# Kernel tuning notes

Measured on AMD Instinct MI355X. Metric: run time of the kernel, lower is better.

Reference implementation:

```python
import jax, jax.numpy as jnp
import numpy as np

EPS_CB = 1e-6   # ConvBlock BN eps (partial(nn.BatchNorm2d, eps=1e-6))
EPS_BN = 1e-5   # default nn.BatchNorm2d / BatchNorm1d eps


def conv2d(x, w, stride=1, pad=0):
    return jax.lax.conv_general_dilated(
        x, w, (stride, stride), [(pad, pad), (pad, pad)],
        dimension_numbers=('NCHW', 'OIHW', 'NCHW'))


def bn2d(x, g, b, m, v, eps):
    inv = (g / jnp.sqrt(v + eps)).reshape(1, -1, 1, 1)
    return (x - m.reshape(1, -1, 1, 1)) * inv + b.reshape(1, -1, 1, 1)


def setup_inputs() -> dict:
    key = jax.random.key(0)
    ks = iter(jax.random.split(key, 40))
    B, C, H, W = 16, 512, 64, 64
    K = 64                 # num_codes (hard-coded to 64 in __init__)
    c4 = C // 4            # bottleneck width in ConvBlock (expansion=4)

    def w_(shape, scale=0.05):
        return jax.random.normal(next(ks), shape, jnp.float32) * scale

    def bnp(n):
        return (jax.random.uniform(next(ks), (n,), jnp.float32, 0.5, 1.5),  # gamma
                w_((n,), 0.05),                                            # beta
                w_((n,), 0.05),                                            # running mean
                jax.random.uniform(next(ks), (n,), jnp.float32, 0.5, 1.5)) # running var

    g1, b1, m1, v1 = bnp(c4)
    g2, b2, m2, v2 = bnp(c4)
    g3, b3, m3, v3 = bnp(C)
    gr, br, mr, vr = bnp(C)
    gl, bl, ml, vl = bnp(C)
    ge, be, me, ve = bnp(K)

    std = 1.0 / np.sqrt(K * C)
    inp = {
        'x': jax.random.normal(next(ks), (B, C, H, W), jnp.float32),
        # ConvBlock
        'w1': w_((c4, C, 1, 1)), 'g1': g1, 'b1': b1, 'm1': m1, 'v1': v1,
        'w2': w_((c4, c4, 3, 3)), 'g2': g2, 'b2': b2, 'm2': m2, 'v2': v2,
        'w3': w_((C, c4, 1, 1)), 'g3': g3, 'b3': b3, 'm3': m3, 'v3': v3,
        'wr': w_((C, C, 1, 1)), 'gr': gr, 'br': br, 'mr': mr, 'vr': vr,
        # LVC 1x1 conv + BN2d
        'wl': w_((C, C, 1, 1)), 'gl': gl, 'bl': bl, 'ml': ml, 'vl': vl,
        # Encoding
        'codewords': jax.random.uniform(next(ks), (K, C), jnp.float32, -std, std),
        'scale': jax.random.uniform(next(ks), (K,), jnp.float32, -1.0, 0.0),
        # BN1d over codes
        'ge': ge, 'be': be, 'me': me, 've': ve,
        # fc gate
        'wfc': w_((C, C)), 'bfc': w_((C,), 0.05),
    }
    return inp


def lvc_forward(x, w1, g1, b1, m1, v1, w2, g2, b2, m2, v2, w3, g3, b3, m3, v3,
                wr, gr, br, mr, vr, wl, gl, bl, ml, vl, codewords, scale,
                ge, be, me, ve, wfc, bfc):
    # ---- ConvBlock (bottleneck with 1x1 residual), eval-mode BN ----
    h = jax.nn.relu(bn2d(conv2d(x, w1), g1, b1, m1, v1, EPS_CB))
    h = jax.nn.relu(bn2d(conv2d(h, w2, pad=1), g2, b2, m2, v2, EPS_CB))
    h = jax.nn.relu(bn2d(conv2d(h, w3), g3, b3, m3, v3, EPS_CB))
    res = bn2d(conv2d(x, wr), gr, br, mr, vr, EPS_CB)
    x1 = h + res                                   # (B, C, H, W)

    # ---- LVC: 1x1 conv + BN + ReLU ----
    y = jax.nn.relu(bn2d(conv2d(x1, wl), gl, bl, ml, vl, EPS_BN))

    # ---- Encoding: scaled L2 -> softmax over codes -> aggregate ----
    B, C, H, W = y.shape
    xf = y.reshape(B, C, H * W).transpose(0, 2, 1)     # (B, N, C)
    x_sq = jnp.sum(xf * xf, axis=-1, keepdims=True)    # (B, N, 1)
    c_sq = jnp.sum(codewords * codewords, axis=-1)     # (K,)
    xc = jnp.einsum('bnc,kc->bnk', xf, codewords)      # (B, N, K)
    dist = scale * (x_sq - 2.0 * xc + c_sq)            # (B, N, K)
    A = jax.nn.softmax(dist, axis=2)                   # assignment weights
    # sum_n A[b,n,k] * (x[b,n,:] - codewords[k,:])  -> (B, K, C)
    enc = jnp.einsum('bnk,bnc->bkc', A, xf) - A.sum(axis=1)[..., None] * codewords

    # ---- BN1d over num_codes dim + ReLU + mean over codes ----
    inv = (ge / jnp.sqrt(ve + EPS_BN)).reshape(1, -1, 1)
    enc = (enc - me.reshape(1, -1, 1)) * inv + be.reshape(1, -1, 1)
    en = jax.nn.relu(enc).mean(axis=1)                 # (B, C)

    # ---- SE-style gate ----
    gam = jax.nn.sigmoid(en @ wfc.T + bfc)             # (B, C)
    gate = gam.reshape(B, C, 1, 1)
    return jax.nn.relu(x1 + x1 * gate)


def reference(x, w1, g1, b1, m1, v1, w2, g2, b2, m2, v2, w3, g3, b3, m3, v3,
              wr, gr, br, mr, vr, wl, gl, bl, ml, vl, codewords, scale,
              ge, be, me, ve, wfc, bfc):
    return lvc_forward(x, w1, g1, b1, m1, v1, w2, g2, b2, m2, v2,
                       w3, g3, b3, m3, v3, wr, gr, br, mr, vr,
                       wl, gl, bl, ml, vl, codewords, scale,
                       ge, be, me, ve, wfc, bfc)
```

## Files before the change

kernel.cpp:

```cpp
#include <hip/hip_runtime.h>
#include <math.h>

typedef float f32x4 __attribute__((ext_vector_type(4)));
typedef short s16x8 __attribute__((ext_vector_type(8)));
typedef unsigned short u16x4 __attribute__((ext_vector_type(4)));

#define HW 4096
#define CCH 512
#define NK 64
#define EPAD 136

#define C_XB   0ULL
#define C_H2   67108864ULL
#define C_H1P  83886080ULL
#define C_X1B  83886080ULL
#define C_YB   0ULL
#define C_AHI  67108864ULL
#define C_ALO  75497472ULL
#define C_ASUM 150994944ULL
#define C_GAM  150999040ULL
#define C_MISC 151031808ULL
#define C_W1F  151048192ULL
#define C_W2F  151179264ULL
#define C_W3B  151474176ULL
#define C_WRB  151605248ULL
#define C_WLB  152129536ULL
#define C_PE   152653824ULL

#define MS_S1 0
#define MS_T1 128
#define MS_S2 256
#define MS_T2 384
#define MS_S3 512
#define MS_T3 1024
#define MS_SR 1536
#define MS_TR 2048
#define MS_SL 2560
#define MS_TL 3072
#define MS_SE 3584
#define MS_TE 3648
#define MS_CSQ 3712

__device__ __forceinline__ float b2f(unsigned short u) {
  unsigned int x = ((unsigned int)u) << 16;
  return __builtin_bit_cast(float, x);
}
__device__ __forceinline__ unsigned short f2b(float f) {
  unsigned int i = __builtin_bit_cast(unsigned int, f);
  i += 0x7fffu + ((i >> 16) & 1u);
  return (unsigned short)(i >> 16);
}

__device__ __forceinline__ void gload16(const void* g, void* l) {
  __builtin_amdgcn_global_load_lds((const __attribute__((address_space(1))) void*)g,
                                   (__attribute__((address_space(3))) void*)l, 16, 0, 0);
}

__global__ void prep_kernel(
    const float* __restrict__ g1, const float* __restrict__ b1, const float* __restrict__ m1, const float* __restrict__ v1,
    const float* __restrict__ g2, const float* __restrict__ b2, const float* __restrict__ m2, const float* __restrict__ v2,
    const float* __restrict__ g3, const float* __restrict__ b3, const float* __restrict__ m3, const float* __restrict__ v3,
    const float* __restrict__ gr, const float* __restrict__ br, const float* __restrict__ mr, const float* __restrict__ vr,
    const float* __restrict__ gl, const float* __restrict__ bl, const float* __restrict__ ml, const float* __restrict__ vl,
    const float* __restrict__ ge, const float* __restrict__ be, const float* __restrict__ me, const float* __restrict__ ve,
    const float* __restrict__ cw, float* __restrict__ misc)
{
  const int t = threadIdx.x;
  if (t < 128) {
    float s = g1[t] * rsqrtf(v1[t] + 1e-6f);
    misc[MS_S1 + t] = s; misc[MS_T1 + t] = b1[t] - m1[t] * s;
    s = g2[t] * rsqrtf(v2[t] + 1e-6f);
    misc[MS_S2 + t] = s; misc[MS_T2 + t] = b2[t] - m2[t] * s;
  }
  for (int c = t; c < 512; c += 256) {
    float s = g3[c] * rsqrtf(v3[c] + 1e-6f);
    misc[MS_S3 + c] = s; misc[MS_T3 + c] = b3[c] - m3[c] * s;
    s = gr[c] * rsqrtf(vr[c] + 1e-6f);
    misc[MS_SR + c] = s; misc[MS_TR + c] = br[c] - mr[c] * s;
    s = gl[c] * rsqrtf(vl[c] + 1e-5f);
    misc[MS_SL + c] = s; misc[MS_TL + c] = bl[c] - ml[c] * s;
  }
  if (t < 64) {
    float s = ge[t] * rsqrtf(ve[t] + 1e-5f);
    misc[MS_SE + t] = s; misc[MS_TE + t] = be[t] - me[t] * s;
    float acc = 0.f;
    for (int c = 0; c < 512; ++c) { float v = cw[t * 512 + c]; acc += v * v; }
    misc[MS_CSQ + t] = acc;
  }
}

__global__ void fold_bf16_kernel(const float* __restrict__ w, const float* __restrict__ s,
                                 unsigned short* __restrict__ out, int total, int kper)
{
  int i = blockIdx.x * 256 + threadIdx.x;
  if (i < total) out[i] = f2b(w[i] * s[i / kper]);
}

__global__ void fold_w2_kernel(const float* __restrict__ w2, const float* __restrict__ s,
                               unsigned short* __restrict__ out)
{
  int j = blockIdx.x * 256 + threadIdx.x;
  if (j < 147456) {
    int m = j / 1152, r = j - m * 1152;
    int tp = r >> 7, ci = r & 127;
    out[j] = f2b(w2[m * 1152 + ci * 9 + tp] * s[m]);
  }
}

__global__ __launch_bounds__(256) void tr_kernel(const float* __restrict__ x,
                                                 unsigned short* __restrict__ xb)
{
  __shared__ float T[64][65];
  const int b = blockIdx.z, c0 = blockIdx.y * 64, n0 = blockIdx.x * 64;
  const int t = threadIdx.x;
  const int rr = t >> 4, cc = (t & 15) * 4;
#pragma unroll
  for (int rep = 0; rep < 4; ++rep) {
    const int cr = rep * 16 + rr;
    const float4 v = *(const float4*)(x + ((size_t)(b * 512 + c0 + cr)) * 4096 + n0 + cc);
    T[cr][cc + 0] = v.x; T[cr][cc + 1] = v.y; T[cr][cc + 2] = v.z; T[cr][cc + 3] = v.w;
  }
  __syncthreads();
#pragma unroll
  for (int rep = 0; rep < 4; ++rep) {
    const int nr = rep * 16 + rr;
    u16x4 o;
    o[0] = f2b(T[cc + 0][nr]); o[1] = f2b(T[cc + 1][nr]);
    o[2] = f2b(T[cc + 2][nr]); o[3] = f2b(T[cc + 3][nr]);
    *(u16x4*)(xb + ((size_t)(b * 4096 + n0 + nr)) * 512 + c0 + cc) = o;
  }
}


__device__ __forceinline__ void mfma_step(const unsigned short* __restrict__ Ac,
                                          const unsigned short* __restrict__ Bc,
                                          int lane, int wm, int wn, f32x4 acc[4][4])
{
  s16x8 afr[4], bfr[4];
#pragma unroll
  for (int i = 0; i < 4; ++i)
    afr[i] = *(const s16x8*)(Ac + (size_t)((wm * 4 + i) * 64 + lane) * 8);
#pragma unroll
  for (int j = 0; j < 4; ++j)
    bfr[j] = *(const s16x8*)(Bc + (size_t)((wn * 4 + j) * 64 + lane) * 8);
#pragma unroll
  for (int i = 0; i < 4; ++i)
#pragma unroll
    for (int j = 0; j < 4; ++j)
      acc[i][j] = __builtin_amdgcn_mfma_f32_16x16x32_bf16(afr[i], bfr[j], acc[i][j], 0, 0, 0);
}

template<int BMODE>
__device__ __forceinline__ void run_phase(
    const unsigned short* __restrict__ Wp,
    const unsigned short* __restrict__ Xb,
    const int K, const int tid, const int n0,
    unsigned short* __restrict__ As, unsigned short* __restrict__ Bs,
    f32x4 acc[4][4])
{
  const int lane = tid & 63;
  const int wv = tid >> 6, wm = wv >> 1, wn = wv & 1;

  const int row0 = (tid >> 6) * 16 + (tid & 15);
  const int row1 = row0 + 64;
  const int kofs = ((tid >> 4) & 3) * 8;

  const unsigned short* aS0 = Wp + (size_t)row0 * K + kofs;
  const unsigned short* aS1 = Wp + (size_t)row1 * K + kofs;

  const unsigned short* bS0 = nullptr;
  const unsigned short* bS1 = nullptr;
  size_t bBase0 = 0, bBase1 = 0;
  if constexpr (BMODE == 0) {
    bS0 = Xb + (size_t)(n0 + row0) * K + kofs;
    bS1 = Xb + (size_t)(n0 + row1) * K + kofs;
  } else {
    const int pg0 = n0 + row0, pg1 = n0 + row1;
    bBase0 = (size_t)((pg0 >> 6) * 66 + (pg0 & 63)) * 128 + kofs;
    bBase1 = (size_t)((pg1 >> 6) * 66 + (pg1 & 63)) * 128 + kofs;
  }

  const int wb = __builtin_amdgcn_readfirstlane(wv * 1024);

#define STAGE(kt, buf)                                            \
  {                                                               \
    char* aD = (char*)As + (buf) * 8192 + wb;                     \
    char* bD = (char*)Bs + (buf) * 8192 + wb;                     \
    if constexpr (BMODE == 0) {                                   \
      gload16(aS0 + (kt), aD);                                    \
      gload16(aS1 + (kt), aD + 4096);                             \
      gload16(bS0 + (kt), bD);                                    \
      gload16(bS1 + (kt), bD + 4096);                             \
    } else {                                                      \
      const int tap_ = (kt) >> 7;                                 \
      const int ky_ = tap_ / 3, kx_ = tap_ - ky_ * 3;             \
      const int off_ = (ky_ * 66 + kx_) * 128 + ((kt) & 127);     \
      gload16(aS0 + (kt), aD);                                    \
      gload16(aS1 + (kt), aD + 4096);                             \
      gload16(Xb + bBase0 + off_, bD);                            \
      gload16(Xb + bBase1 + off_, bD + 4096);                     \
    }                                                             \
  }

  STAGE(0, 0);
  __syncthreads();

  int cur = 0;
  for (int kt = 0; kt < K; kt += 32) {
    if (kt + 32 < K) STAGE(kt + 32, cur ^ 1);
    mfma_step(As + cur * 4096, Bs + cur * 4096, lane, wm, wn, acc);
    __syncthreads();
    cur ^= 1;
  }
#undef STAGE
}

template<int BMODE, bool DUAL>
__global__ __launch_bounds__(256) void mgemm_kernel(
    const unsigned short* __restrict__ W0, const unsigned short* __restrict__ X0,
    const int K0, const long long xbs0,
    const unsigned short* __restrict__ W1, const unsigned short* __restrict__ X1,
    const int Kp1, const long long xbs1,
    const float* __restrict__ biasMid, const float* __restrict__ biasOut,
    const int omode, const int reluF, const int ldm,
    unsigned short* __restrict__ outB, const long long obsB)
{
  __shared__ __align__(16) unsigned short smem[128 * EPAD];
  unsigned short* As = smem;
  unsigned short* Bs = smem + 8192;

  const int tid = threadIdx.x;
  const int b = blockIdx.z;
  const int n0 = blockIdx.x * 128;
  const int m0 = blockIdx.y * 128;
  const int lane = tid & 63, wv = tid >> 6, wm = wv >> 1, wn = wv & 1;
  const int q = lane >> 4, mm = lane & 15;

  f32x4 acc[4][4];
#pragma unroll
  for (int i = 0; i < 4; ++i)
#pragma unroll
    for (int j = 0; j < 4; ++j) acc[i][j] = (f32x4){0.f, 0.f, 0.f, 0.f};

  run_phase<BMODE>(W0 + (size_t)m0 * K0, X0 + (size_t)b * xbs0, K0, tid, n0, As, Bs, acc);

  if constexpr (DUAL) {
#pragma unroll
    for (int i = 0; i < 4; ++i) {
      const int mb = m0 + wm * 64 + i * 16 + q * 4;
#pragma unroll
      for (int r = 0; r < 4; ++r) {
        const float bm = biasMid[mb + r];
#pragma unroll
        for (int j = 0; j < 4; ++j) acc[i][j][r] = fmaxf(acc[i][j][r] + bm, 0.f);
      }
    }
    run_phase<0>(W1 + (size_t)m0 * Kp1, X1 + (size_t)b * xbs1, Kp1, tid, n0, As, Bs, acc);
  }

  __syncthreads();
  if (omode == 3) {
#pragma unroll
    for (int i = 0; i < 4; ++i) {
      const int chb = wm * 64 + i * 16 + q * 4;
#pragma unroll
      for (int r = 0; r < 4; ++r) {
        const float bo = biasOut[m0 + chb + r];
#pragma unroll
        for (int j = 0; j < 4; ++j) {
          const int px = wn * 64 + j * 16 + mm;
          float v = acc[i][j][r] + bo;
          if (reluF) v = fmaxf(v, 0.f);
          smem[(size_t)(chb + r) * EPAD + px] = f2b(v);
        }
      }
    }
    __syncthreads();
    const int ch = tid >> 1, half = tid & 1;
    const unsigned short* src = smem + (size_t)ch * EPAD + half * 64;
    unsigned short* dst = outB + (size_t)b * obsB + (size_t)(m0 + ch) * HW + n0 + half * 64;
#pragma unroll
    for (int r = 0; r < 8; ++r) {
      s16x8 v;
      __builtin_memcpy(&v, src + r * 8, 16);
      *(s16x8*)(dst + r * 8) = v;
    }
  } else {
#pragma unroll
    for (int i = 0; i < 4; ++i) {
      const int chb = wm * 64 + i * 16 + q * 4;
      float bo[4];
#pragma unroll
      for (int r = 0; r < 4; ++r) bo[r] = biasOut[m0 + chb + r];
#pragma unroll
      for (int j = 0; j < 4; ++j) {
        const int px = wn * 64 + j * 16 + mm;
        u16x4 o;
#pragma unroll
        for (int r = 0; r < 4; ++r) {
          float v = acc[i][j][r] + bo[r];
          if (reluF) v = fmaxf(v, 0.f);
          o[r] = f2b(v);
        }
        *(u16x4*)(smem + (size_t)px * EPAD + chb) = o;
      }
    }
    __syncthreads();
    const int px = tid >> 1, half = tid & 1;
    const unsigned short* src = smem + (size_t)px * EPAD + half * 64;
    size_t dstoff;
    if (omode == 1) {
      dstoff = (size_t)b * obsB + (size_t)(n0 + px) * ldm + m0 + half * 64;
    } else {
      const int hp = ((n0 + px) >> 6) + 1, wp = ((n0 + px) & 63) + 1;
      dstoff = (size_t)b * obsB + ((size_t)hp * 66 + wp) * 128 + m0 + half * 64;
    }
    unsigned short* dst = outB + dstoff;
#pragma unroll
    for (int r = 0; r < 8; ++r) {
      s16x8 v;
      __builtin_memcpy(&v, src + r * 8, 16);
      *(s16x8*)(dst + r * 8) = v;
    }
  }
}

__global__ __launch_bounds__(256) void assign_kernel(
    const unsigned short* __restrict__ Yv, const float* __restrict__ cw, const float* __restrict__ scale,
    const float* __restrict__ misc, unsigned short* __restrict__ Ahi, unsigned short* __restrict__ Alo)
{
  __shared__ float Cs[16][64];
  __shared__ float Ys[16][64];
  __shared__ float dist[64][65];
  __shared__ float red[4][64];
  __shared__ float xsq[64];
  __shared__ float scl[64];
  __shared__ float csq[64];
  const int tid = threadIdx.x;
  const int b  = blockIdx.y;
  const int n0 = blockIdx.x * 64;
  if (tid < 64) { scl[tid] = scale[tid]; csq[tid] = misc[MS_CSQ + tid]; }
  const unsigned short* __restrict__ Yb = Yv + (size_t)b * CCH * HW;
  const int tr = tid >> 4, tc = tid & 15;
  const int lc_k = tid >> 2, lc_c = (tid & 3) * 4;
  const int ly_c0 = tid >> 6, ly_n = tid & 63;

  float acc[4][4];
#pragma unroll
  for (int i = 0; i < 4; ++i)
#pragma unroll
    for (int j = 0; j < 4; ++j) acc[i][j] = 0.f;
  float sq = 0.f;

  for (int c0 = 0; c0 < 512; c0 += 16) {
    const float4 cv = *(const float4*)(cw + (size_t)lc_k * 512 + c0 + lc_c);
    float yv[4];
#pragma unroll
    for (int rr = 0; rr < 4; ++rr)
      yv[rr] = b2f(Yb[(size_t)(c0 + ly_c0 + rr * 4) * HW + n0 + ly_n]);
    __syncthreads();
    Cs[lc_c + 0][lc_k] = cv.x;
    Cs[lc_c + 1][lc_k] = cv.y;
    Cs[lc_c + 2][lc_k] = cv.z;
    Cs[lc_c + 3][lc_k] = cv.w;
#pragma unroll
    for (int rr = 0; rr < 4; ++rr) {
      Ys[ly_c0 + rr * 4][ly_n] = yv[rr];
      sq += yv[rr] * yv[rr];
    }
    __syncthreads();
#pragma unroll
    for (int ct = 0; ct < 16; ++ct) {
      float rk[4], rn[4];
#pragma unroll
      for (int i = 0; i < 4; ++i) rk[i] = Cs[ct][tr * 4 + i];
#pragma unroll
      for (int j = 0; j < 4; ++j) rn[j] = Ys[ct][tc * 4 + j];
#pragma unroll
      for (int i = 0; i < 4; ++i)
#pragma unroll
        for (int j = 0; j < 4; ++j) acc[i][j] += rk[i] * rn[j];
    }
  }
  __syncthreads();
  red[ly_c0][ly_n] = sq;
  __syncthreads();
  if (tid < 64) xsq[tid] = red[0][tid] + red[1][tid] + red[2][tid] + red[3][tid];
  __syncthreads();
#pragma unroll
  for (int i = 0; i < 4; ++i)
#pragma unroll
    for (int j = 0; j < 4; ++j) {
      const int k = tr * 4 + i, n = tc * 4 + j;
      dist[k][n] = scl[k] * (xsq[n] - 2.f * acc[i][j] + csq[k]);
    }
  __syncthreads();
  const int qq = tid >> 6, n = tid & 63;
  float mx = -3.0e38f;
#pragma unroll
  for (int kk = 0; kk < 16; ++kk) mx = fmaxf(mx, dist[qq * 16 + kk][n]);
  red[qq][n] = mx;
  __syncthreads();
  mx = fmaxf(fmaxf(red[0][n], red[1][n]), fmaxf(red[2][n], red[3][n]));
  __syncthreads();
  float sum = 0.f;
#pragma unroll
  for (int kk = 0; kk < 16; ++kk) {
    const float e = __expf(dist[qq * 16 + kk][n] - mx);
    dist[qq * 16 + kk][n] = e;
    sum += e;
  }
  red[qq][n] = sum;
  __syncthreads();
  sum = red[0][n] + red[1][n] + red[2][n] + red[3][n];
  const float inv = 1.f / sum;
  const size_t base = (size_t)b * NK * HW + n0 + n;
#pragma unroll
  for (int kk = 0; kk < 16; ++kk) {
    const float a = dist[qq * 16 + kk][n] * inv;
    const unsigned short hi = f2b(a);
    const float rem = a - b2f(hi);
    Ahi[base + (size_t)(qq * 16 + kk) * HW] = hi;
    Alo[base + (size_t)(qq * 16 + kk) * HW] = f2b(rem);
  }
}

__global__ void asum_kernel(const unsigned short* __restrict__ Ahi,
                            const unsigned short* __restrict__ Alo, float* __restrict__ asum)
{
  const int bk = blockIdx.x;
  const unsigned short* __restrict__ rh = Ahi + (size_t)bk * HW;
  const unsigned short* __restrict__ rl = Alo + (size_t)bk * HW;
  const int t = threadIdx.x;
  float p = 0.f;
  for (int i = t * 8; i < HW; i += 2048) {
    s16x8 h, l;
    __builtin_memcpy(&h, rh + i, 16);
    __builtin_memcpy(&l, rl + i, 16);
#pragma unroll
    for (int e = 0; e < 8; ++e)
      p += b2f((unsigned short)h[e]) + b2f((unsigned short)l[e]);
  }
  __shared__ float sm[256];
  sm[t] = p;
  __syncthreads();
  for (int s = 128; s > 0; s >>= 1) {
    if (t < s) sm[t] += sm[t + s];
    __syncthreads();
  }
  if (t == 0) asum[bk] = sm[0];
}

__global__ __launch_bounds__(256) void enc_mfma_kernel(
    const unsigned short* __restrict__ Ahi, const unsigned short* __restrict__ Alo,
    const unsigned short* __restrict__ Yv, float* __restrict__ pe)
{
  __shared__ __align__(16) unsigned short AHs[2048];
  __shared__ __align__(16) unsigned short ALs[2048];
  __shared__ __align__(16) unsigned short Bs[4096];
  const int tid = threadIdx.x;
  const int ncol = blockIdx.x, nc = blockIdx.y, b = blockIdx.z;
  const int lane = tid & 63, wv = tid >> 6;
  const int q = lane >> 4, mm = lane & 15;

  const int ko = tid & 3;
  const int r  = tid >> 2;
  const size_t aoff = ((size_t)b * NK + r) * HW + nc * 1024 + ko * 8;
  const unsigned short* ahS = Ahi + aoff;
  const unsigned short* alS = Alo + aoff;
  const int slotA = (((r >> 4) * 64) + ko * 16 + (r & 15)) * 8;
  const unsigned short* b0S = Yv + ((size_t)b * CCH + ncol * 128 + r) * HW + nc * 1024 + ko * 8;
  const unsigned short* b1S = b0S + (size_t)64 * HW;
  const int slotB0 = (((r >> 4) * 64) + ko * 16 + (r & 15)) * 8;
  const int slotB1 = ((((r + 64) >> 4) * 64) + ko * 16 + (r & 15)) * 8;

  f32x4 acc[4][2];
#pragma unroll
  for (int i = 0; i < 4; ++i)
#pragma unroll
    for (int j = 0; j < 2; ++j) acc[i][j] = (f32x4){0.f, 0.f, 0.f, 0.f};

  for (int kt = 0; kt < 1024; kt += 32) {
    s16x8 ah, al, y0, y1;
    __builtin_memcpy(&ah, ahS + kt, 16);
    __builtin_memcpy(&al, alS + kt, 16);
    __builtin_memcpy(&y0, b0S + kt, 16);
    __builtin_memcpy(&y1, b1S + kt, 16);
    __syncthreads();
    *(s16x8*)(AHs + slotA) = ah;
    *(s16x8*)(ALs + slotA) = al;
    *(s16x8*)(Bs + slotB0) = y0;
    *(s16x8*)(Bs + slotB1) = y1;
    __syncthreads();

    s16x8 afh[4], afl[4], bfr[2];
#pragma unroll
    for (int i = 0; i < 4; ++i) {
      afh[i] = *(const s16x8*)(AHs + (size_t)(i * 64 + lane) * 8);
      afl[i] = *(const s16x8*)(ALs + (size_t)(i * 64 + lane) * 8);
    }
#pragma unroll
    for (int j = 0; j < 2; ++j)
      bfr[j] = *(const s16x8*)(Bs + (size_t)((wv * 2 + j) * 64 + lane) * 8);
#pragma unroll
    for (int i = 0; i < 4; ++i)
#pragma unroll
      for (int j = 0; j < 2; ++j) {
        acc[i][j] = __builtin_amdgcn_mfma_f32_16x16x32_bf16(afh[i], bfr[j], acc[i][j], 0, 0, 0);
        acc[i][j] = __builtin_amdgcn_mfma_f32_16x16x32_bf16(afl[i], bfr[j], acc[i][j], 0, 0, 0);
      }
  }

  float* __restrict__ peb = pe + ((size_t)(b * 4 + nc) * NK) * CCH;
#pragma unroll
  for (int i = 0; i < 4; ++i)
#pragma unroll
    for (int j = 0; j < 2; ++j) {
      const int c = ncol * 128 + (wv * 2 + j) * 16 + mm;
#pragma unroll
      for (int rr = 0; rr < 4; ++rr) {
        const int k = i * 16 + q * 4 + rr;
        peb[(size_t)k * CCH + c] = acc[i][j][rr];
      }
    }
}

__global__ __launch_bounds__(256) void engate_kernel(
    const float* __restrict__ pe, const float* __restrict__ asum, const float* __restrict__ cw,
    const float* __restrict__ misc, const float* __restrict__ wfc, const float* __restrict__ bfc,
    float* __restrict__ gam)
{
  const int b = blockIdx.x;
  const int t = threadIdx.x;
  __shared__ float asum_s[64], se_s[64], te_s[64];
  __shared__ __align__(16) float en_s[512];
  if (t < 64) {
    asum_s[t] = asum[b * 64 + t];
    se_s[t]   = misc[MS_SE + t];
    te_s[t]   = misc[MS_TE + t];
  }
  __syncthreads();
  for (int rep = 0; rep < 2; ++rep) {
    const int c = t + rep * 256;
    float en = 0.f;
    const float* __restrict__ peb = pe + (size_t)b * 4 * NK * CCH + c;
    for (int k = 0; k < 64; ++k) {
      const float ps = peb[(size_t)k * CCH] + peb[(size_t)(64 + k) * CCH] +
                       peb[(size_t)(128 + k) * CCH] + peb[(size_t)(192 + k) * CCH];
      float v = ps - asum_s[k] * cw[k * 512 + c];
      v = v * se_s[k] + te_s[k];
      en += fmaxf(v, 0.f);
    }
    en_s[c] = en * (1.f / 64.f);
  }
  __syncthreads();
  for (int rep = 0; rep < 2; ++rep) {
    const int i = t + rep * 256;
    float a = bfc[i];
    const float4* __restrict__ wrow = (const float4*)(wfc + (size_t)i * 512);
    const float4* __restrict__ ev = (const float4*)en_s;
    for (int j = 0; j < 128; ++j) {
      const float4 w4 = wrow[j];
      const float4 e4 = ev[j];
      a += w4.x * e4.x + w4.y * e4.y + w4.z * e4.z + w4.w * e4.w;
    }
    gam[b * 512 + i] = 1.f / (1.f + __expf(-a));
  }
}

__global__ __launch_bounds__(256) void fingate_kernel(
    const unsigned short* __restrict__ x1b, const float* __restrict__ gam,
    float* __restrict__ out)
{
  __shared__ float T[64][65];
  const int b = blockIdx.z, c0 = blockIdx.y * 64, n0 = blockIdx.x * 64;
  const int t = threadIdx.x;
  const int rr = t >> 4, cc = (t & 15) * 4;
#pragma unroll
  for (int rep = 0; rep < 4; ++rep) {
    const int pr = rep * 16 + rr;
    u16x4 v = *(const u16x4*)(x1b + ((size_t)(b * 4096 + n0 + pr)) * 512 + c0 + cc);
    T[cc + 0][pr] = b2f(v[0]);
    T[cc + 1][pr] = b2f(v[1]);
    T[cc + 2][pr] = b2f(v[2]);
    T[cc + 3][pr] = b2f(v[3]);
  }
  __syncthreads();
#pragma unroll
  for (int rep = 0; rep < 4; ++rep) {
    const int cr = rep * 16 + rr;
    const float g = 1.f + gam[b * 512 + c0 + cr];
    float4 o;
    o.x = fmaxf(T[cr][cc + 0] * g, 0.f);
    o.y = fmaxf(T[cr][cc + 1] * g, 0.f);
    o.z = fmaxf(T[cr][cc + 2] * g, 0.f);
    o.w = fmaxf(T[cr][cc + 3] * g, 0.f);
    *(float4*)(out + ((size_t)(b * 512 + c0 + cr)) * 4096 + n0 + cc) = o;
  }
}

extern "C" void kernel_launch(void* const* d_in, const int* in_sizes, int n_in,
                              void* d_out, int out_size, void* d_ws, size_t ws_size,
                              hipStream_t stream)
{
  const float* x  = (const float*)d_in[0];
  const float* w1 = (const float*)d_in[1];
  const float* g1 = (const float*)d_in[2];
  const float* b1 = (const float*)d_in[3];
  const float* m1 = (const float*)d_in[4];
  const float* v1 = (const float*)d_in[5];
  const float* w2 = (const float*)d_in[6];
  const float* g2 = (const float*)d_in[7];
  const float* b2 = (const float*)d_in[8];
  const float* m2 = (const float*)d_in[9];
  const float* v2 = (const float*)d_in[10];
  const float* w3 = (const float*)d_in[11];
  const float* g3 = (const float*)d_in[12];
  const float* b3 = (const float*)d_in[13];
  const float* m3 = (const float*)d_in[14];
  const float* v3 = (const float*)d_in[15];
  const float* wr = (const float*)d_in[16];
  const float* gr = (const float*)d_in[17];
  const float* br = (const float*)d_in[18];
  const float* mr = (const float*)d_in[19];
  const float* vr = (const float*)d_in[20];
  const float* wl = (const float*)d_in[21];
  const float* gl = (const float*)d_in[22];
  const float* bl = (const float*)d_in[23];
  const float* ml = (const float*)d_in[24];
  const float* vl = (const float*)d_in[25];
  const float* cw = (const float*)d_in[26];
  const float* scale = (const float*)d_in[27];
  const float* ge = (const float*)d_in[28];
  const float* be = (const float*)d_in[29];
  const float* me = (const float*)d_in[30];
  const float* ve = (const float*)d_in[31];
  const float* wfc = (const float*)d_in[32];
  const float* bfc = (const float*)d_in[33];

  char* wsb = (char*)d_ws;
  unsigned short* xb  = (unsigned short*)(wsb + C_XB);
  unsigned short* h2  = (unsigned short*)(wsb + C_H2);
  unsigned short* h1p = (unsigned short*)(wsb + C_H1P);
  unsigned short* x1b = (unsigned short*)(wsb + C_X1B);
  unsigned short* yb  = (unsigned short*)(wsb + C_YB);
  unsigned short* Ahi = (unsigned short*)(wsb + C_AHI);
  unsigned short* Alo = (unsigned short*)(wsb + C_ALO);
  float* pe   = (float*)(wsb + C_PE);
  float* asum = (float*)(wsb + C_ASUM);
  float* gam  = (float*)(wsb + C_GAM);
  float* misc = (float*)(wsb + C_MISC);
  unsigned short* w1f = (unsigned short*)(wsb + C_W1F);
  unsigned short* w2f = (unsigned short*)(wsb + C_W2F);
  unsigned short* w3b = (unsigned short*)(wsb + C_W3B);
  unsigned short* wrb = (unsigned short*)(wsb + C_WRB);
  unsigned short* wlb = (unsigned short*)(wsb + C_WLB);

  prep_kernel<<<1, 256, 0, stream>>>(g1, b1, m1, v1, g2, b2, m2, v2, g3, b3, m3, v3,
                                     gr, br, mr, vr, gl, bl, ml, vl, ge, be, me, ve,
                                     cw, misc);
  fold_bf16_kernel<<<256, 256, 0, stream>>>(w1, misc + MS_S1, w1f, 65536, 512);
  fold_w2_kernel<<<576, 256, 0, stream>>>(w2, misc + MS_S2, w2f);
  fold_bf16_kernel<<<256, 256, 0, stream>>>(w3, misc + MS_S3, w3b, 65536, 128);
  fold_bf16_kernel<<<1024, 256, 0, stream>>>(wr, misc + MS_SR, wrb, 262144, 512);
  fold_bf16_kernel<<<1024, 256, 0, stream>>>(wl, misc + MS_SL, wlb, 262144, 512);

  tr_kernel<<<dim3(64, 8, 16), 256, 0, stream>>>(x, xb);
  hipMemsetAsync(h1p, 0, 17842176, stream);

  mgemm_kernel<0, false><<<dim3(32, 1, 16), 256, 0, stream>>>(
      w1f, xb, 512, 4096LL * 512, nullptr, nullptr, 0, 0,
      nullptr, misc + MS_T1, 0, 1, 128, h1p, 4356LL * 128);
  mgemm_kernel<1, false><<<dim3(32, 1, 16), 256, 0, stream>>>(
      w2f, h1p, 1152, 4356LL * 128, nullptr, nullptr, 0, 0,
      nullptr, misc + MS_T2, 1, 1, 128, h2, 4096LL * 128);
  mgemm_kernel<0, true><<<dim3(32, 4, 16), 256, 0, stream>>>(
      w3b, h2, 128, 4096LL * 128, wrb, xb, 512, 4096LL * 512,
      misc + MS_T3, misc + MS_TR, 1, 0, 512, x1b, 4096LL * 512);
  mgemm_kernel<0, false><<<dim3(32, 4, 16), 256, 0, stream>>>(
      wlb, x1b, 512, 4096LL * 512, nullptr, nullptr, 0, 0,
      nullptr, misc + MS_TL, 3, 1, 0, yb, 512LL * 4096);

  assign_kernel<<<dim3(64, 16), 256, 0, stream>>>(yb, cw, scale, misc, Ahi, Alo);
  asum_kernel<<<1024, 256, 0, stream>>>(Ahi, Alo, asum);
  enc_mfma_kernel<<<dim3(4, 4, 16), 256, 0, stream>>>(Ahi, Alo, yb, pe);
  engate_kernel<<<16, 256, 0, stream>>>(pe, asum, cw, misc, wfc, bfc, gam);
  fingate_kernel<<<dim3(64, 8, 16), 256, 0, stream>>>(x1b, gam, (float*)d_out);
}
```

Baseline: 493.1 us.

## Deepen GEMM shared-memory pipeline to three stages with partial vmcnt waits

Replaces the double-buffered A/B staging in the MFMA GEMM main loop with a triple-buffered ring in a single shared array. Loads are issued two k-tiles ahead, and each iteration waits only on the oldest tile via partial s_waitcnt vmcnt instead of draining all loads at a __syncthreads. The goal is to hide global-load latency behind MFMA work. In exchange, each iteration now has two raw barriers and the shared-memory footprint grows, which may reduce blocks per CU.

```diff
diff --git a/kernel.cpp b/kernel.cpp
--- a/kernel.cpp
+++ b/kernel.cpp
@@ -155,7 +155,7 @@
     const unsigned short* __restrict__ Wp,
     const unsigned short* __restrict__ Xb,
     const int K, const int tid, const int n0,
-    unsigned short* __restrict__ As, unsigned short* __restrict__ Bs,
+    unsigned short* __restrict__ Sm,
     f32x4 acc[4][4])
 {
   const int lane = tid & 63;
@@ -184,8 +184,8 @@
 
 #define STAGE(kt, buf)                                            \
   {                                                               \
-    char* aD = (char*)As + (buf) * 8192 + wb;                     \
-    char* bD = (char*)Bs + (buf) * 8192 + wb;                     \
+    char* aD = (char*)Sm + (buf) * 16384 + wb;                    \
+    char* bD = (char*)Sm + (buf) * 16384 + 8192 + wb;             \
     if constexpr (BMODE == 0) {                                   \
       gload16(aS0 + (kt), aD);                                    \
       gload16(aS1 + (kt), aD + 4096);                             \
@@ -202,15 +202,27 @@
     }                                                             \
   }
 
+  const int NC = K >> 5;
   STAGE(0, 0);
-  __syncthreads();
+  STAGE(32, 1);
 
   int cur = 0;
-  for (int kt = 0; kt < K; kt += 32) {
-    if (kt + 32 < K) STAGE(kt + 32, cur ^ 1);
-    mfma_step(As + cur * 4096, Bs + cur * 4096, lane, wm, wn, acc);
-    __syncthreads();
-    cur ^= 1;
+  for (int c = 0; c < NC; ++c) {
+    const int stg = c + 2;
+    if (stg < NC) {
+      STAGE(stg * 32, stg % 3);
+      asm volatile("s_waitcnt vmcnt(8)" ::: "memory");
+    } else if (c + 1 < NC) {
+      asm volatile("s_waitcnt vmcnt(4)" ::: "memory");
+    } else {
+      asm volatile("s_waitcnt vmcnt(0)" ::: "memory");
+    }
+    __builtin_amdgcn_s_barrier();
+    asm volatile("" ::: "memory");
+    mfma_step(Sm + cur * 8192, Sm + cur * 8192 + 4096, lane, wm, wn, acc);
+    asm volatile("" ::: "memory");
+    __builtin_amdgcn_s_barrier();
+    cur = (cur == 2) ? 0 : cur + 1;
   }
 #undef STAGE
 }
@@ -225,10 +237,7 @@
     const int omode, const int reluF, const int ldm,
     unsigned short* __restrict__ outB, const long long obsB)
 {
-  __shared__ __align__(16) unsigned short smem[128 * EPAD];
-  unsigned short* As = smem;
-  unsigned short* Bs = smem + 8192;
-
+  __shared__ __align__(16) unsigned short smem[24576];
   const int tid = threadIdx.x;
   const int b = blockIdx.z;
   const int n0 = blockIdx.x * 128;
@@ -242,7 +251,7 @@
 #pragma unroll
     for (int j = 0; j < 4; ++j) acc[i][j] = (f32x4){0.f, 0.f, 0.f, 0.f};
 
-  run_phase<BMODE>(W0 + (size_t)m0 * K0, X0 + (size_t)b * xbs0, K0, tid, n0, As, Bs, acc);
+  run_phase<BMODE>(W0 + (size_t)m0 * K0, X0 + (size_t)b * xbs0, K0, tid, n0, smem, acc);
 
   if constexpr (DUAL) {
 #pragma unroll
@@ -255,7 +264,7 @@
         for (int j = 0; j < 4; ++j) acc[i][j][r] = fmaxf(acc[i][j][r] + bm, 0.f);
       }
     }
-    run_phase<0>(W1 + (size_t)m0 * Kp1, X1 + (size_t)b * xbs1, Kp1, tid, n0, As, Bs, acc);
+    run_phase<0>(W1 + (size_t)m0 * Kp1, X1 + (size_t)b * xbs1, Kp1, tid, n0, smem, acc);
   }
 
   __syncthreads();
```

After: 480.4 us. -2.6%, faster.
